# Kernel optimization log

Hardware: AMD Instinct MI355X
Metric: run time of the kernel (lower is better)

Reference implementation:

```python
import jax, jax.numpy as jnp
import numpy as np

B, S, D = 4, 2048, 768
H, E = 12, 64  # num_heads, head_size


def setup_inputs() -> dict:
    key = jax.random.key(0)
    ks = jax.random.split(key, 9)
    sd = 1.0 / np.sqrt(D)
    return {
        "x": jax.random.normal(ks[0], (B, S, D), dtype=jnp.float32),
        "Wq": jax.random.normal(ks[1], (H, D, E), dtype=jnp.float32) * sd,
        "bq": jax.random.normal(ks[2], (H, E), dtype=jnp.float32) * 0.02,
        "Wk": jax.random.normal(ks[3], (H, D, E), dtype=jnp.float32) * sd,
        "bk": jax.random.normal(ks[4], (H, E), dtype=jnp.float32) * 0.02,
        "Wv": jax.random.normal(ks[5], (H, D, E), dtype=jnp.float32) * sd,
        "bv": jax.random.normal(ks[6], (H, E), dtype=jnp.float32) * 0.02,
        "Wp": jax.random.normal(ks[7], (H * E, D), dtype=jnp.float32) * sd,
        "bp": jax.random.normal(ks[8], (D,), dtype=jnp.float32) * 0.02,
    }


def reference(x, Wq, bq, Wk, bk, Wv, bv, Wp, bp):
    # Batched multi-head QKV projections (replaces per-head Python loop)
    q = jnp.einsum("bsd,hde->bhse", x, Wq) + bq[None, :, None, :]
    k = jnp.einsum("bsd,hde->bhse", x, Wk) + bk[None, :, None, :]
    v = jnp.einsum("bsd,hde->bhse", x, Wv) + bv[None, :, None, :]
    scale = 1.0 / jnp.sqrt(jnp.asarray(E, dtype=x.dtype))
    # Full materialized attention matrix [B,H,S,S] as in the original module
    wei = jnp.einsum("bhqe,bhke->bhqk", q, k) * scale
    wei = jax.nn.softmax(wei, axis=-1)  # dropout=0 (eval) => identity
    out = jnp.einsum("bhqk,bhke->bhqe", wei, v)  # [B,H,S,E]
    # concat heads in head order then output projection
    out = out.transpose(0, 2, 1, 3).reshape(B, S, H * E)
    return out @ Wp + bp
```

## Files before the change

kernel.cpp:

```cpp
#include <hip/hip_runtime.h>
#include <cstddef>
#include <cstdint>

#define NB 4
#define NH 12
#define SQ 2048
#define DM 768
#define EH 64
#define MTOT (NB*SQ)
#define NQKV (NH*3*EH)

typedef __attribute__((ext_vector_type(8))) short short8;
typedef __attribute__((ext_vector_type(4))) float floatx4;

#define QSCALE 0.18033688011112042f

__device__ __forceinline__ unsigned short f2bf(float f) {
    unsigned int u = __float_as_uint(f);
    u += 0x7fffu + ((u >> 16) & 1u);
    return (unsigned short)(u >> 16);
}

#if __has_builtin(__builtin_amdgcn_exp2f)
__device__ __forceinline__ float fast_exp2(float x) { return __builtin_amdgcn_exp2f(x); }
#else
__device__ __forceinline__ float fast_exp2(float x) { return exp2f(x); }
#endif

#if __has_builtin(__builtin_amdgcn_cvt_pk_bf16_f32)
typedef __attribute__((ext_vector_type(2))) __bf16 bf16x2_t;
__device__ __forceinline__ unsigned int pack_bf16(float lo, float hi) {
    bf16x2_t v = __builtin_amdgcn_cvt_pk_bf16_f32(lo, hi);
    return __builtin_bit_cast(unsigned int, v);
}
#else
__device__ __forceinline__ unsigned int pack_bf16(float lo, float hi) {
    unsigned int u0 = __float_as_uint(lo) + 0x8000u;
    unsigned int u1 = __float_as_uint(hi) + 0x8000u;
    return __builtin_amdgcn_perm(u1, u0, 0x07060302u);
}
#endif
__device__ __forceinline__ short8 pack8(float a0,float a1,float a2,float a3,
                                        float b0,float b1,float b2,float b3) {
    union { unsigned int u[4]; short8 s; } cv;
    cv.u[0] = pack_bf16(a0, a1);
    cv.u[1] = pack_bf16(a2, a3);
    cv.u[2] = pack_bf16(b0, b1);
    cv.u[3] = pack_bf16(b2, b3);
    return cv.s;
}
__device__ __forceinline__ void gl_lds16(const void* g, void* l) {
    __builtin_amdgcn_global_load_lds(
        (const __attribute__((address_space(1))) unsigned int*)g,
        (__attribute__((address_space(3))) unsigned int*)l, 16, 0, 0);
}

#define CVT_A 1572864
#define CVT_B (CVT_A + 442368)
#define CVT_C (CVT_B + 147456)
#define CVT_D (CVT_C + 576)
__global__ __launch_bounds__(256) void convert_pack(
    const float* __restrict__ x,
    const float* __restrict__ Wq, const float* __restrict__ bq,
    const float* __restrict__ Wk, const float* __restrict__ bk,
    const float* __restrict__ Wv, const float* __restrict__ bv,
    const float* __restrict__ Wp,
    unsigned short* __restrict__ Xb, unsigned short* __restrict__ Wt,
    unsigned short* __restrict__ Wpt, float* __restrict__ bias_all)
{
    int t = blockIdx.x * 256 + threadIdx.x;
    if (t < CVT_A) {
        float4 v = ((const float4*)x)[t];
        ushort4 r; r.x = f2bf(v.x); r.y = f2bf(v.y); r.z = f2bf(v.z); r.w = f2bf(v.w);
        ((ushort4*)Xb)[t] = r;
    } else if (t < CVT_B) {
        int u = t - CVT_A;
        int n = u / 192, kc = (u % 192) * 4;
        int h = n / 192, rr = n % 192, wsel = rr >> 6, e = rr & 63;
        const float* W = (wsel == 0) ? Wq : ((wsel == 1) ? Wk : Wv);
        float sc = (wsel == 0) ? QSCALE : 1.0f;
        ushort4 r;
        r.x = f2bf(W[((size_t)h * DM + kc + 0) * EH + e] * sc);
        r.y = f2bf(W[((size_t)h * DM + kc + 1) * EH + e] * sc);
        r.z = f2bf(W[((size_t)h * DM + kc + 2) * EH + e] * sc);
        r.w = f2bf(W[((size_t)h * DM + kc + 3) * EH + e] * sc);
        ((ushort4*)Wt)[u] = r;
    } else if (t < CVT_C) {
        int u = t - CVT_B;
        int n = u / 192, kc = (u % 192) * 4;
        ushort4 r;
        r.x = f2bf(Wp[(size_t)(kc + 0) * DM + n]);
        r.y = f2bf(Wp[(size_t)(kc + 1) * DM + n]);
        r.z = f2bf(Wp[(size_t)(kc + 2) * DM + n]);
        r.w = f2bf(Wp[(size_t)(kc + 3) * DM + n]);
        ((ushort4*)Wpt)[u] = r;
    } else if (t < CVT_D) {
        int u = (t - CVT_C) * 4;
        #pragma unroll
        for (int j = 0; j < 4; j++) {
            int n = u + j;
            int h = n / 192, rr = n % 192, wsel = rr >> 6, e = rr & 63;
            const float* bs = (wsel == 0) ? bq : ((wsel == 1) ? bk : bv);
            bias_all[n] = bs[h * EH + e] * ((wsel == 0) ? QSCALE : 1.0f);
        }
    }
}

__global__ __launch_bounds__(256) void qkv_mfma(
    const unsigned short* __restrict__ Xb, const unsigned short* __restrict__ Wt,
    const float* __restrict__ bias_all,
    unsigned short* __restrict__ Qo, unsigned short* __restrict__ Kf,
    unsigned short* __restrict__ Vf)
{
    __shared__ unsigned short As[2][128 * 32];
    __shared__ unsigned short Bs[2][128 * 32];
    __shared__ unsigned short Ep[4][16 * 72];
    const int tid = threadIdx.x;
    const int w = tid >> 6, lane = tid & 63;
    const int l15 = lane & 15, quad = lane >> 4;
    const int wm = w & 1, wn = w >> 1;
    const int m0 = blockIdx.x * 128, n0 = blockIdx.y * 128;
    const int srow = w * 32 + (lane >> 2);
    const int pchunk = lane & 3;

    floatx4 acc[4][4];
    #pragma unroll
    for (int i = 0; i < 4; i++)
        #pragma unroll
        for (int j = 0; j < 4; j++) acc[i][j] = 0;

    #pragma unroll
    for (int c = 0; c < 2; c++) {
        int mr = srow + c * 16;
        int j = (pchunk - (mr >> 1)) & 3;
        gl_lds16(&Xb[(size_t)(m0 + mr) * DM + j * 8],
                 &As[0][w * 1024 + c * 512 + lane * 8]);
        gl_lds16(&Wt[(size_t)(n0 + mr) * DM + j * 8],
                 &Bs[0][w * 1024 + c * 512 + lane * 8]);
    }

    for (int kt = 0; kt < DM / 32; kt++) {
        const int cur = kt & 1;
        __syncthreads();
        if (kt + 1 < DM / 32) {
            int k0n = (kt + 1) * 32;
            #pragma unroll
            for (int c = 0; c < 2; c++) {
                int mr = srow + c * 16;
                int j = (pchunk - (mr >> 1)) & 3;
                gl_lds16(&Xb[(size_t)(m0 + mr) * DM + k0n + j * 8],
                         &As[cur ^ 1][w * 1024 + c * 512 + lane * 8]);
                gl_lds16(&Wt[(size_t)(n0 + mr) * DM + k0n + j * 8],
                         &Bs[cur ^ 1][w * 1024 + c * 512 + lane * 8]);
            }
        }
        short8 af[4], bf[4];
        #pragma unroll
        for (int mi = 0; mi < 4; mi++) {
            int row = wm * 64 + mi * 16 + l15;
            int pp = (quad + (row >> 1)) & 3;
            af[mi] = *(const short8*)&As[cur][row * 32 + pp * 8];
        }
        #pragma unroll
        for (int ni = 0; ni < 4; ni++) {
            int row = wn * 64 + ni * 16 + l15;
            int pp = (quad + (row >> 1)) & 3;
            bf[ni] = *(const short8*)&Bs[cur][row * 32 + pp * 8];
        }
        #pragma unroll
        for (int mi = 0; mi < 4; mi++)
            #pragma unroll
            for (int ni = 0; ni < 4; ni++)
                acc[mi][ni] = __builtin_amdgcn_mfma_f32_16x16x32_bf16(
                    af[mi], bf[ni], acc[mi][ni], 0, 0, 0);
    }
    __syncthreads();

    const int bB = m0 >> 11;
    const int ntb0 = n0 + wn * 64;
    const int h = ntb0 / 192, rr = ntb0 % 192;
    const int wsel = rr >> 6;
    const size_t bhbase = ((size_t)bB * NH + h) * (SQ * EH);
    const int sb_base = (m0 & 2047) + wm * 64;
    unsigned short* Ew = &Ep[w][0];
    float bvv[4];
    #pragma unroll
    for (int ni = 0; ni < 4; ni++) bvv[ni] = bias_all[ntb0 + ni * 16 + l15];

    if (wsel == 0) {
        #pragma unroll
        for (int mi = 0; mi < 4; mi++) {
            #pragma unroll
            for (int ni = 0; ni < 4; ni++)
                #pragma unroll
                for (int r = 0; r < 4; r++)
                    Ew[(quad * 4 + r) * 72 + ni * 16 + l15] =
                        f2bf(acc[mi][ni][r] + bvv[ni]);
            #pragma unroll
            for (int t = 0; t < 2; t++) {
                uint4 d = *(uint4*)&Ew[(t * 8 + (lane >> 3)) * 72 + (lane & 7) * 8];
                *(uint4*)&Qo[bhbase +
                    (size_t)(sb_base + mi * 16 + t * 8 + (lane >> 3)) * EH +
                    (lane & 7) * 8] = d;
            }
        }
    } else if (wsel == 1) {
        size_t tbase = bhbase + (size_t)(sb_base >> 6) * 4096;
        #pragma unroll
        for (int mi = 0; mi < 4; mi++) {
            #pragma unroll
            for (int ni = 0; ni < 4; ni++)
                #pragma unroll
                for (int r = 0; r < 4; r++)
                    Ew[(quad * 4 + r) * 72 + ni * 16 + l15] =
                        f2bf(acc[mi][ni][r] + bvv[ni]);
            #pragma unroll
            for (int t = 0; t < 2; t++) {
                uint4 d = *(uint4*)&Ew[l15 * 72 + t * 32 + quad * 8];
                *(uint4*)&Kf[tbase +
                    (size_t)((mi * 2 + t) * 64 + quad * 16 + l15) * 8] = d;
            }
        }
    } else {
        size_t tbase = bhbase + (size_t)(sb_base >> 6) * 4096;
        #pragma unroll
        for (int ni = 0; ni < 4; ni++) {
            #pragma unroll
            for (int mi = 0; mi < 4; mi++)
                #pragma unroll
                for (int r = 0; r < 4; r += 2) {
                    unsigned int pr = pack_bf16(acc[mi][ni][r]     + bvv[ni],
                                                acc[mi][ni][r + 1] + bvv[ni]);
                    *(unsigned int*)&Ew[l15 * 72 + quad * 16 + mi * 4 + r] = pr;
                }
            #pragma unroll
            for (int t = 0; t < 2; t++) {
                uint4 d = *(uint4*)&Ew[l15 * 72 + t * 32 + quad * 8];
                int unit = (ni * 2 + (quad & 1)) * 64 + ((quad >> 1) + 2 * t) * 16 + l15;
                *(uint4*)&Vf[tbase + (size_t)unit * 8] = d;
            }
        }
    }
}

__global__ __launch_bounds__(256, 3) void attn_mfma(
    const unsigned short* __restrict__ Q, const unsigned short* __restrict__ Kf,
    const unsigned short* __restrict__ Vf, unsigned short* __restrict__ O)
{
    __shared__ unsigned short Ks[3 * 4096];
    __shared__ unsigned short Vs[3 * 4096];
    const int tid = threadIdx.x;
    const int w = tid >> 6, lane = tid & 63;
    const int l15 = lane & 15, quad = lane >> 4;
    const int bh = blockIdx.x;
    const int b = bh / NH, h = bh % NH;
    const int q0 = blockIdx.y * 128;

    const unsigned short* Qb = Q + (size_t)bh * SQ * EH;
    const unsigned short* Kb = Kf + (size_t)bh * SQ * EH;
    const unsigned short* Vb = Vf + (size_t)bh * SQ * EH;

    short8 qf[2][2];
    #pragma unroll
    for (int qh = 0; qh < 2; qh++)
        #pragma unroll
        for (int kh = 0; kh < 2; kh++)
            qf[qh][kh] = *(const short8*)
                &Qb[(size_t)(q0 + w * 32 + qh * 16 + l15) * EH + kh * 32 + quad * 8];

    short8 ones;
    #pragma unroll
    for (int j = 0; j < 8; j++) ones[j] = (short)0x3F80;
    const floatx4 fzero = 0;

    floatx4 o[2][4], l_acc[2];
    #pragma unroll
    for (int qh = 0; qh < 2; qh++) {
        l_acc[qh] = 0;
        #pragma unroll
        for (int nb = 0; nb < 4; nb++) o[qh][nb] = 0;
    }

    const int seg = w * 2;
    #pragma unroll
    for (int c = 0; c < 2; c++) {
        gl_lds16(&Kb[(seg + c) * 512 + lane * 8], &Ks[(seg + c) * 512 + lane * 8]);
        gl_lds16(&Vb[(seg + c) * 512 + lane * 8], &Vs[(seg + c) * 512 + lane * 8]);
    }
    asm volatile("" ::: "memory");
    #pragma unroll
    for (int c = 0; c < 2; c++) {
        gl_lds16(&Kb[4096 + (seg + c) * 512 + lane * 8],
                 &Ks[4096 + (seg + c) * 512 + lane * 8]);
        gl_lds16(&Vb[4096 + (seg + c) * 512 + lane * 8],
                 &Vs[4096 + (seg + c) * 512 + lane * 8]);
    }
    asm volatile("s_waitcnt vmcnt(4)\n\ts_barrier" ::: "memory");

    int cur_off = 0;
    for (int kb = 0; kb < SQ / 64; kb++) {
        if (kb + 2 < SQ / 64) {
            int nxt_off = cur_off + 8192;
            if (nxt_off >= 12288) nxt_off -= 12288;
            const unsigned short* Kn = Kb + (size_t)(kb + 2) * 4096;
            const unsigned short* Vn = Vb + (size_t)(kb + 2) * 4096;
            #pragma unroll
            for (int c = 0; c < 2; c++) {
                gl_lds16(&Kn[(seg + c) * 512 + lane * 8],
                         &Ks[nxt_off + (seg + c) * 512 + lane * 8]);
                gl_lds16(&Vn[(seg + c) * 512 + lane * 8],
                         &Vs[nxt_off + (seg + c) * 512 + lane * 8]);
            }
        }

        short8 kf[4][2], vf[4][2];
        #pragma unroll
        for (int nb = 0; nb < 4; nb++)
            #pragma unroll
            for (int kh = 0; kh < 2; kh++)
                kf[nb][kh] = *(const short8*)&Ks[cur_off + ((nb * 2 + kh) * 64 + lane) * 8];
        #pragma unroll
        for (int eb = 0; eb < 4; eb++)
            #pragma unroll
            for (int kh = 0; kh < 2; kh++)
                vf[eb][kh] = *(const short8*)&Vs[cur_off + ((eb * 2 + kh) * 64 + lane) * 8];

        floatx4 s[2][4];
        __builtin_amdgcn_s_setprio(1);
        #pragma unroll
        for (int qh = 0; qh < 2; qh++)
            #pragma unroll
            for (int nb = 0; nb < 4; nb++) {
                floatx4 z = __builtin_amdgcn_mfma_f32_16x16x32_bf16(
                    kf[nb][0], qf[qh][0], fzero, 0, 0, 0);
                s[qh][nb] = __builtin_amdgcn_mfma_f32_16x16x32_bf16(
                    kf[nb][1], qf[qh][1], z, 0, 0, 0);
            }
        __builtin_amdgcn_s_setprio(0);

        short8 pa[2][2];
        #pragma unroll
        for (int qh = 0; qh < 2; qh++) {
            float p[4][4];
            #pragma unroll
            for (int nb = 0; nb < 4; nb++)
                #pragma unroll
                for (int r = 0; r < 4; r++)
                    p[nb][r] = fast_exp2(s[qh][nb][r]);
            pa[qh][0] = pack8(p[0][0], p[0][1], p[0][2], p[0][3],
                              p[1][0], p[1][1], p[1][2], p[1][3]);
            pa[qh][1] = pack8(p[2][0], p[2][1], p[2][2], p[2][3],
                              p[3][0], p[3][1], p[3][2], p[3][3]);
        }

        __builtin_amdgcn_s_setprio(1);
        #pragma unroll
        for (int qh = 0; qh < 2; qh++) {
            l_acc[qh] = __builtin_amdgcn_mfma_f32_16x16x32_bf16(pa[qh][0], ones, l_acc[qh], 0, 0, 0);
            l_acc[qh] = __builtin_amdgcn_mfma_f32_16x16x32_bf16(pa[qh][1], ones, l_acc[qh], 0, 0, 0);
        }
        #pragma unroll
        for (int qh = 0; qh < 2; qh++)
            #pragma unroll
            for (int eb = 0; eb < 4; eb++) {
                o[qh][eb] = __builtin_amdgcn_mfma_f32_16x16x32_bf16(pa[qh][0], vf[eb][0], o[qh][eb], 0, 0, 0);
                o[qh][eb] = __builtin_amdgcn_mfma_f32_16x16x32_bf16(pa[qh][1], vf[eb][1], o[qh][eb], 0, 0, 0);
            }
        __builtin_amdgcn_s_setprio(0);

        if (kb + 2 < SQ / 64) {
            asm volatile("s_waitcnt vmcnt(4)\n\ts_barrier" ::: "memory");
        } else if (kb + 1 < SQ / 64) {
            asm volatile("s_waitcnt vmcnt(0)\n\ts_barrier" ::: "memory");
        }
        cur_off += 4096;
        if (cur_off >= 12288) cur_off = 0;
    }

    #pragma unroll
    for (int qh = 0; qh < 2; qh++)
        #pragma unroll
        for (int r = 0; r < 4; r++) {
            float inv = 1.0f / l_acc[qh][r];
            int sidx = q0 + w * 32 + qh * 16 + quad * 4 + r;
            size_t base = (((size_t)b * SQ + sidx) * NH + h) * EH + l15;
            O[base +  0] = f2bf(o[qh][0][r] * inv);
            O[base + 16] = f2bf(o[qh][1][r] * inv);
            O[base + 32] = f2bf(o[qh][2][r] * inv);
            O[base + 48] = f2bf(o[qh][3][r] * inv);
        }
}

__global__ __launch_bounds__(256) void proj_mfma(
    const unsigned short* __restrict__ Ab, const unsigned short* __restrict__ Wpt,
    const float* __restrict__ bp, float* __restrict__ C)
{
    __shared__ unsigned short As[2][64 * 32];
    __shared__ unsigned short Bs[2][128 * 32];
    __shared__ float Epf[4][16 * 68];
    const int tid = threadIdx.x;
    const int w = tid >> 6, lane = tid & 63;
    const int l15 = lane & 15, quad = lane >> 4;
    const int wm = w & 1, wn = w >> 1;
    const int m0 = blockIdx.x * 64, n0 = blockIdx.y * 128;
    const int pchunk = lane & 3;

    floatx4 acc[2][4];
    #pragma unroll
    for (int i = 0; i < 2; i++)
        #pragma unroll
        for (int j = 0; j < 4; j++) acc[i][j] = 0;

    {
        int mr = w * 16 + (lane >> 2);
        int j = (pchunk - (mr >> 1)) & 3;
        gl_lds16(&Ab[(size_t)(m0 + mr) * DM + j * 8], &As[0][w * 512 + lane * 8]);
    }
    #pragma unroll
    for (int c = 0; c < 2; c++) {
        int nr = w * 32 + c * 16 + (lane >> 2);
        int j = (pchunk - (nr >> 1)) & 3;
        gl_lds16(&Wpt[(size_t)(n0 + nr) * DM + j * 8],
                 &Bs[0][w * 1024 + c * 512 + lane * 8]);
    }

    for (int kt = 0; kt < DM / 32; kt++) {
        const int cur = kt & 1;
        __syncthreads();
        if (kt + 1 < DM / 32) {
            int k0n = (kt + 1) * 32;
            {
                int mr = w * 16 + (lane >> 2);
                int j = (pchunk - (mr >> 1)) & 3;
                gl_lds16(&Ab[(size_t)(m0 + mr) * DM + k0n + j * 8],
                         &As[cur ^ 1][w * 512 + lane * 8]);
            }
            #pragma unroll
            for (int c = 0; c < 2; c++) {
                int nr = w * 32 + c * 16 + (lane >> 2);
                int j = (pchunk - (nr >> 1)) & 3;
                gl_lds16(&Wpt[(size_t)(n0 + nr) * DM + k0n + j * 8],
                         &Bs[cur ^ 1][w * 1024 + c * 512 + lane * 8]);
            }
        }
        short8 af[2], bf[4];
        #pragma unroll
        for (int mi = 0; mi < 2; mi++) {
            int row = wm * 32 + mi * 16 + l15;
            int pp = (quad + (row >> 1)) & 3;
            af[mi] = *(const short8*)&As[cur][row * 32 + pp * 8];
        }
        #pragma unroll
        for (int ni = 0; ni < 4; ni++) {
            int row = wn * 64 + ni * 16 + l15;
            int pp = (quad + (row >> 1)) & 3;
            bf[ni] = *(const short8*)&Bs[cur][row * 32 + pp * 8];
        }
        #pragma unroll
        for (int mi = 0; mi < 2; mi++)
            #pragma unroll
            for (int ni = 0; ni < 4; ni++)
                acc[mi][ni] = __builtin_amdgcn_mfma_f32_16x16x32_bf16(
                    af[mi], bf[ni], acc[mi][ni], 0, 0, 0);
    }
    __syncthreads();

    float* Ewf = &Epf[w][0];
    float bvv[4];
    #pragma unroll
    for (int ni = 0; ni < 4; ni++) bvv[ni] = bp[n0 + wn * 64 + ni * 16 + l15];
    #pragma unroll
    for (int mi = 0; mi < 2; mi++) {
        #pragma unroll
        for (int ni = 0; ni < 4; ni++)
            #pragma unroll
            for (int r = 0; r < 4; r++)
                Ewf[(quad * 4 + r) * 68 + ni * 16 + l15] = acc[mi][ni][r] + bvv[ni];
        #pragma unroll
        for (int t = 0; t < 4; t++) {
            float4 d = *(float4*)&Ewf[(t * 4 + quad) * 68 + l15 * 4];
            *(float4*)&C[(size_t)(m0 + wm * 32 + mi * 16 + t * 4 + quad) * DM +
                         n0 + wn * 64 + l15 * 4] = d;
        }
    }
}

extern "C" void kernel_launch(void* const* d_in, const int* in_sizes, int n_in,
                              void* d_out, int out_size, void* d_ws, size_t ws_size,
                              hipStream_t stream) {
    const float* x  = (const float*)d_in[0];
    const float* Wq = (const float*)d_in[1];
    const float* bq = (const float*)d_in[2];
    const float* Wk = (const float*)d_in[3];
    const float* bk = (const float*)d_in[4];
    const float* Wv = (const float*)d_in[5];
    const float* bv = (const float*)d_in[6];
    const float* Wp = (const float*)d_in[7];
    const float* bp = (const float*)d_in[8];
    float* out = (float*)d_out;

    const size_t QKV_ELEMS = (size_t)NB * NH * SQ * EH;
    unsigned short* Qb   = (unsigned short*)d_ws;
    unsigned short* Kfb  = Qb + QKV_ELEMS;
    unsigned short* Vfb  = Kfb + QKV_ELEMS;
    unsigned short* Abuf = Vfb + QKV_ELEMS;
    unsigned short* Xb   = Abuf + QKV_ELEMS;
    unsigned short* Wtb  = Xb + QKV_ELEMS;
    unsigned short* Wptb = Wtb + (size_t)NQKV * DM;
    float* bias_all      = (float*)(Wptb + (size_t)DM * DM);

    convert_pack<<<(CVT_D + 255) / 256, 256, 0, stream>>>(
        x, Wq, bq, Wk, bk, Wv, bv, Wp, Xb, Wtb, Wptb, bias_all);
    qkv_mfma<<<dim3(MTOT / 128, NQKV / 128), 256, 0, stream>>>(
        Xb, Wtb, bias_all, Qb, Kfb, Vfb);
    attn_mfma<<<dim3(NB * NH, SQ / 128), 256, 0, stream>>>(Qb, Kfb, Vfb, Abuf);
    proj_mfma<<<dim3(MTOT / 64, DM / 128), 256, 0, stream>>>(Abuf, Wptb, bp, out);
}
```

Measured before the change: 230.4 us.

## Software-pipeline attention loop so QK^T of next block overlaps exp and PV

Restructures the attention inner loop into a prologue, steady state and epilogue. Each iteration issues the QK^T MFMAs for block t+1 together with the PV MFMAs for block t, then computes exp on the new scores afterwards. The goal is to overlap the transcendental exp work with matrix-core work instead of running them back to back. In exchange, the wait before each barrier changes from vmcnt(4) to vmcnt(0), which may expose more load latency, and register pressure rises because the scores and probabilities stay live across stages.

```diff
diff --git a/kernel.cpp b/kernel.cpp
--- a/kernel.cpp
+++ b/kernel.cpp
@@ -287,7 +287,6 @@
         gl_lds16(&Kb[(seg + c) * 512 + lane * 8], &Ks[(seg + c) * 512 + lane * 8]);
         gl_lds16(&Vb[(seg + c) * 512 + lane * 8], &Vs[(seg + c) * 512 + lane * 8]);
     }
-    asm volatile("" ::: "memory");
     #pragma unroll
     for (int c = 0; c < 2; c++) {
         gl_lds16(&Kb[4096 + (seg + c) * 512 + lane * 8],
@@ -295,38 +294,17 @@
         gl_lds16(&Vb[4096 + (seg + c) * 512 + lane * 8],
                  &Vs[4096 + (seg + c) * 512 + lane * 8]);
     }
-    asm volatile("s_waitcnt vmcnt(4)\n\ts_barrier" ::: "memory");
-
-    int cur_off = 0;
-    for (int kb = 0; kb < SQ / 64; kb++) {
-        if (kb + 2 < SQ / 64) {
-            int nxt_off = cur_off + 8192;
-            if (nxt_off >= 12288) nxt_off -= 12288;
-            const unsigned short* Kn = Kb + (size_t)(kb + 2) * 4096;
-            const unsigned short* Vn = Vb + (size_t)(kb + 2) * 4096;
-            #pragma unroll
-            for (int c = 0; c < 2; c++) {
-                gl_lds16(&Kn[(seg + c) * 512 + lane * 8],
-                         &Ks[nxt_off + (seg + c) * 512 + lane * 8]);
-                gl_lds16(&Vn[(seg + c) * 512 + lane * 8],
-                         &Vs[nxt_off + (seg + c) * 512 + lane * 8]);
-            }
-        }
-
-        short8 kf[4][2], vf[4][2];
+    asm volatile("s_waitcnt vmcnt(0)\n\ts_barrier" ::: "memory");
+
+    short8 pa[2][2];
+    {
+        short8 kf[4][2];
         #pragma unroll
         for (int nb = 0; nb < 4; nb++)
             #pragma unroll
             for (int kh = 0; kh < 2; kh++)
-                kf[nb][kh] = *(const short8*)&Ks[cur_off + ((nb * 2 + kh) * 64 + lane) * 8];
-        #pragma unroll
-        for (int eb = 0; eb < 4; eb++)
-            #pragma unroll
-            for (int kh = 0; kh < 2; kh++)
-                vf[eb][kh] = *(const short8*)&Vs[cur_off + ((eb * 2 + kh) * 64 + lane) * 8];
-
+                kf[nb][kh] = *(const short8*)&Ks[((nb * 2 + kh) * 64 + lane) * 8];
         floatx4 s[2][4];
-        __builtin_amdgcn_s_setprio(1);
         #pragma unroll
         for (int qh = 0; qh < 2; qh++)
             #pragma unroll
@@ -336,9 +314,6 @@
                 s[qh][nb] = __builtin_amdgcn_mfma_f32_16x16x32_bf16(
                     kf[nb][1], qf[qh][1], z, 0, 0, 0);
             }
-        __builtin_amdgcn_s_setprio(0);
-
-        short8 pa[2][2];
         #pragma unroll
         for (int qh = 0; qh < 2; qh++) {
             float p[4][4];
@@ -352,8 +327,44 @@
             pa[qh][1] = pack8(p[2][0], p[2][1], p[2][2], p[2][3],
                               p[3][0], p[3][1], p[3][2], p[3][3]);
         }
-
+    }
+
+    int offV = 0, offK = 4096, offS = 8192;
+    for (int t = 0; t < SQ / 64 - 1; t++) {
+        if (t < SQ / 64 - 2) {
+            const unsigned short* Kn = Kb + (size_t)(t + 2) * 4096;
+            const unsigned short* Vn = Vb + (size_t)(t + 2) * 4096;
+            #pragma unroll
+            for (int c = 0; c < 2; c++) {
+                gl_lds16(&Kn[(seg + c) * 512 + lane * 8],
+                         &Ks[offS + (seg + c) * 512 + lane * 8]);
+                gl_lds16(&Vn[(seg + c) * 512 + lane * 8],
+                         &Vs[offS + (seg + c) * 512 + lane * 8]);
+            }
+        }
+        short8 kf[4][2];
+        #pragma unroll
+        for (int nb = 0; nb < 4; nb++)
+            #pragma unroll
+            for (int kh = 0; kh < 2; kh++)
+                kf[nb][kh] = *(const short8*)&Ks[offK + ((nb * 2 + kh) * 64 + lane) * 8];
+        floatx4 s[2][4];
         __builtin_amdgcn_s_setprio(1);
+        #pragma unroll
+        for (int qh = 0; qh < 2; qh++)
+            #pragma unroll
+            for (int nb = 0; nb < 4; nb++) {
+                floatx4 z = __builtin_amdgcn_mfma_f32_16x16x32_bf16(
+                    kf[nb][0], qf[qh][0], fzero, 0, 0, 0);
+                s[qh][nb] = __builtin_amdgcn_mfma_f32_16x16x32_bf16(
+                    kf[nb][1], qf[qh][1], z, 0, 0, 0);
+            }
+        short8 vf[4][2];
+        #pragma unroll
+        for (int eb = 0; eb < 4; eb++)
+            #pragma unroll
+            for (int kh = 0; kh < 2; kh++)
+                vf[eb][kh] = *(const short8*)&Vs[offV + ((eb * 2 + kh) * 64 + lane) * 8];
         #pragma unroll
         for (int qh = 0; qh < 2; qh++) {
             l_acc[qh] = __builtin_amdgcn_mfma_f32_16x16x32_bf16(pa[qh][0], ones, l_acc[qh], 0, 0, 0);
@@ -367,14 +378,42 @@
                 o[qh][eb] = __builtin_amdgcn_mfma_f32_16x16x32_bf16(pa[qh][1], vf[eb][1], o[qh][eb], 0, 0, 0);
             }
         __builtin_amdgcn_s_setprio(0);
-
-        if (kb + 2 < SQ / 64) {
-            asm volatile("s_waitcnt vmcnt(4)\n\ts_barrier" ::: "memory");
-        } else if (kb + 1 < SQ / 64) {
-            asm volatile("s_waitcnt vmcnt(0)\n\ts_barrier" ::: "memory");
-        }
-        cur_off += 4096;
-        if (cur_off >= 12288) cur_off = 0;
+        #pragma unroll
+        for (int qh = 0; qh < 2; qh++) {
+            float p[4][4];
+            #pragma unroll
+            for (int nb = 0; nb < 4; nb++)
+                #pragma unroll
+                for (int r = 0; r < 4; r++)
+                    p[nb][r] = fast_exp2(s[qh][nb][r]);
+            pa[qh][0] = pack8(p[0][0], p[0][1], p[0][2], p[0][3],
+                              p[1][0], p[1][1], p[1][2], p[1][3]);
+            pa[qh][1] = pack8(p[2][0], p[2][1], p[2][2], p[2][3],
+                              p[3][0], p[3][1], p[3][2], p[3][3]);
+        }
+        asm volatile("s_waitcnt vmcnt(0)\n\ts_barrier" ::: "memory");
+        int tmp = offV; offV = offK; offK = offS; offS = tmp;
+    }
+
+    {
+        short8 vf[4][2];
+        #pragma unroll
+        for (int eb = 0; eb < 4; eb++)
+            #pragma unroll
+            for (int kh = 0; kh < 2; kh++)
+                vf[eb][kh] = *(const short8*)&Vs[offV + ((eb * 2 + kh) * 64 + lane) * 8];
+        #pragma unroll
+        for (int qh = 0; qh < 2; qh++) {
+            l_acc[qh] = __builtin_amdgcn_mfma_f32_16x16x32_bf16(pa[qh][0], ones, l_acc[qh], 0, 0, 0);
+            l_acc[qh] = __builtin_amdgcn_mfma_f32_16x16x32_bf16(pa[qh][1], ones, l_acc[qh], 0, 0, 0);
+        }
+        #pragma unroll
+        for (int qh = 0; qh < 2; qh++)
+            #pragma unroll
+            for (int eb = 0; eb < 4; eb++) {
+                o[qh][eb] = __builtin_amdgcn_mfma_f32_16x16x32_bf16(pa[qh][0], vf[eb][0], o[qh][eb], 0, 0, 0);
+                o[qh][eb] = __builtin_amdgcn_mfma_f32_16x16x32_bf16(pa[qh][1], vf[eb][1], o[qh][eb], 0, 0, 0);
+            }
     }
 
     #pragma unroll
```

Result: no change. 232.3 us (+0.8%).
